# Kernel optimization log

Measured on AMD Instinct MI355X. Metric: run time of the kernel, lower is better.

Reference implementation:

```python
import jax, jax.numpy as jnp
import numpy as np

N_NODES = 100000
N_EDGES = 1600000
N_GRAPHS = 1024
HID = 128
NODE_DIM = 7
EDGE_DIM = 3
LAYERS = 4
LN_EPS = 1e-5


def setup_inputs() -> dict:
    key = jax.random.key(0)
    ks = jax.random.split(key, 24)
    s = lambda i, shape, scale=0.05: (jax.random.normal(ks[i], shape, dtype=jnp.float32) * scale)
    x = jax.random.normal(ks[0], (N_NODES, NODE_DIM), dtype=jnp.float32)
    edge_index = jax.random.randint(ks[1], (2, N_EDGES), 0, N_NODES, dtype=jnp.int32)
    edge_attr = jax.random.normal(ks[2], (N_EDGES, EDGE_DIM), dtype=jnp.float32)
    batch = jnp.sort(jax.random.randint(ks[3], (N_NODES,), 0, N_GRAPHS, dtype=jnp.int32))
    return {
        'x': x, 'edge_index': edge_index, 'edge_attr': edge_attr, 'batch': batch,
        'inW': s(4, (NODE_DIM, HID)), 'inb': s(5, (HID,)),
        'edgeW': s(6, (LAYERS, EDGE_DIM, HID)), 'edgeb': s(7, (LAYERS, HID)),
        'w1': s(8, (LAYERS, HID, HID)), 'b1': s(9, (LAYERS, HID)),
        'w2': s(10, (LAYERS, HID, HID)), 'b2': s(11, (LAYERS, HID)),
        'gamma': jnp.ones((LAYERS, HID), dtype=jnp.float32),
        'beta': jnp.zeros((LAYERS, HID), dtype=jnp.float32),
        'fcW1': s(12, (HID, HID)), 'fcb1': s(13, (HID,)),
        'fcW2': s(14, (HID, HID // 2)), 'fcb2': s(15, (HID // 2,)),
        'fcW3': s(16, (HID // 2, 1)), 'fcb3': s(17, (1,)),
    }


def _layernorm(x, gamma, beta):
    mu = jnp.mean(x, axis=-1, keepdims=True)
    var = jnp.mean(jnp.square(x - mu), axis=-1, keepdims=True)
    return (x - mu) * jax.lax.rsqrt(var + LN_EPS) * gamma + beta


def reference(x, edge_index, edge_attr, batch, inW, inb, edgeW, edgeb,
              w1, b1, w2, b2, gamma, beta, fcW1, fcb1, fcW2, fcb2, fcW3, fcb3):
    src, dst = edge_index[0], edge_index[1]
    h = x @ inW + inb  # [N, HID]
    for l in range(LAYERS):
        e = edge_attr @ edgeW[l] + edgeb[l]              # [E, HID]
        msg = jax.nn.relu(h[src] + e)                    # gather + relu
        agg = jax.ops.segment_sum(msg, dst, num_segments=N_NODES)  # scatter-add
        g = agg + h                                      # (1+eps)*x_r with eps=0
        g = jax.nn.relu(g @ w1[l] + b1[l]) @ w2[l] + b2[l]  # GINE MLP
        h = _layernorm(h + jax.nn.relu(g), gamma[l], beta[l])  # residual + LN
    # global mean pool over graphs
    sums = jax.ops.segment_sum(h, batch, num_segments=N_GRAPHS)
    cnt = jax.ops.segment_sum(jnp.ones((h.shape[0],), h.dtype), batch, num_segments=N_GRAPHS)
    pooled = sums / jnp.maximum(cnt, 1.0)[:, None]
    # head (dropout is identity in eval)
    o = jax.nn.relu(pooled @ fcW1 + fcb1)
    o = jax.nn.relu(o @ fcW2 + fcb2)
    return o @ fcW3 + fcb3  # [N_GRAPHS, 1]
```

## Files before the change

kernel.cpp:

```cpp
#include <hip/hip_runtime.h>

#define N_NODES 100000
#define N_EDGES 1600000
#define N_GRAPHS 1024
#define HID 128
#define LAYERS 4
#define LN_EPS 1e-5f
#define GTS 136
#define HLS 132
#define NB_PROJ 50000
#define NB_WCONV 512
#define NBUCK 1563
#define BCAP 2048
#define NSTREAM 8
#define CURPAD 32
#define EPB 4096
#define NB_BS 391


typedef __attribute__((ext_vector_type(8))) short bf16x8;
typedef __attribute__((ext_vector_type(4))) float f32x4;
typedef __attribute__((ext_vector_type(2))) float f32x2;

__device__ __forceinline__ unsigned short f2bf(float x) {
    unsigned v = __float_as_uint(x);
    return (unsigned short)((v + 0x7fffu + ((v >> 16) & 1u)) >> 16);
}
__device__ __forceinline__ float bfval(unsigned short u) {
    return __uint_as_float((unsigned)u << 16);
}
__device__ __forceinline__ f32x2 pk_fma(f32x2 a, f32x2 b, f32x2 c) {
    f32x2 d;
    asm("v_pk_fma_f32 %0, %1, %2, %3" : "=v"(d) : "v"(a), "v"(b), "v"(c));
    return d;
}
__device__ __forceinline__ f32x2 pk_add(f32x2 a, f32x2 b) {
    f32x2 d;
    asm("v_pk_add_f32 %0, %1, %2" : "=v"(d) : "v"(a), "v"(b));
    return d;
}

__global__ __launch_bounds__(256) void k_prep(
    const float* __restrict__ x, const float* __restrict__ inW,
    const float* __restrict__ inb, float* __restrict__ h,
    unsigned short* __restrict__ hb,
    const float* __restrict__ w1, const float* __restrict__ w2,
    unsigned short* __restrict__ wf_hi, unsigned short* __restrict__ wf_lo) {
    if (blockIdx.x < NB_PROJ) {
        int idx = blockIdx.x * 256 + threadIdx.x;
        int n = idx >> 7, c = idx & 127;
        const float* xr = x + n * 7;
        float s = inb[c];
#pragma unroll
        for (int k = 0; k < 7; ++k) s += xr[k] * inW[k * HID + c];
        h[idx] = s;
        hb[idx] = f2bf(s);
    } else {
        int idx = (blockIdx.x - NB_PROJ) * 256 + threadIdx.x;
        int wid = idx >> 14;
        int layer = wid >> 1, which = wid & 1;
        int within = idx & 16383;
        int nt = within >> 11;
        int ks = (within >> 9) & 3;
        int ln = (within >> 3) & 63;
        int j = within & 7;
        const float* W = (which ? w2 : w1) + layer * HID * HID;
        int k = ks * 32 + (ln >> 4) * 8 + j;
        int n = nt * 16 + (ln & 15);
        float v = W[k * HID + n];
        unsigned short hi = f2bf(v);
        wf_hi[idx] = hi;
        wf_lo[idx] = f2bf(v - bfval(hi));
    }
}

__global__ __launch_bounds__(256) void k_hist(
    const int* __restrict__ ei, int* __restrict__ cnt2) {
    __shared__ int hcnt[NBUCK];
    const int t = threadIdx.x;
    for (int i = t; i < NBUCK; i += 256) hcnt[i] = 0;
    __syncthreads();
    const int e0 = blockIdx.x * EPB;
    const int eend = (e0 + EPB < N_EDGES) ? e0 + EPB : N_EDGES;
#pragma unroll
    for (int k = 0; k < 16; ++k) {
        const int e = e0 + k * 256 + t;
        if (e < eend) atomicAdd(&hcnt[ei[N_EDGES + e] >> 6], 1);
    }
    __syncthreads();
    const int sgrp = blockIdx.x & 7;
    for (int i = t; i < NBUCK; i += 256) {
        const int c = hcnt[i];
        if (c) atomicAdd(&cnt2[((i << 3) + sgrp) << 5], c);
    }
}

__global__ __launch_bounds__(1024) void k_segscan(
    const int* __restrict__ cnt2, int* __restrict__ pcur,
    int* __restrict__ bucket_base, int* __restrict__ row_ptr) {
    __shared__ int lsum[1024];
    const int t = threadIdx.x;
    const int b0 = 2 * t, b1 = 2 * t + 1;
    int u0 = 0, u1 = 0;
    if (b0 < NBUCK) {
#pragma unroll
        for (int s = 0; s < NSTREAM; ++s) u0 += cnt2[((b0 << 3) + s) << 5];
    }
    if (b1 < NBUCK) {
#pragma unroll
        for (int s = 0; s < NSTREAM; ++s) u1 += cnt2[((b1 << 3) + s) << 5];
    }
    const int v = u0 + u1;
    lsum[t] = v;
    __syncthreads();
    for (int off = 1; off < 1024; off <<= 1) {
        const int u = (t >= off) ? lsum[t - off] : 0;
        __syncthreads();
        lsum[t] += u;
        __syncthreads();
    }
    const int excl = lsum[t] - v;
    if (b0 < NBUCK) {
        bucket_base[b0] = excl;
        int run = excl;
#pragma unroll
        for (int s = 0; s < NSTREAM; ++s) {
            const int c = ((b0 << 3) + s) << 5;
            pcur[c] = run;
            run += cnt2[c];
        }
    }
    if (b1 < NBUCK) {
        const int base1 = excl + u0;
        bucket_base[b1] = base1;
        int run = base1;
#pragma unroll
        for (int s = 0; s < NSTREAM; ++s) {
            const int c = ((b1 << 3) + s) << 5;
            pcur[c] = run;
            run += cnt2[c];
        }
    }
    if (t == 0) {
        bucket_base[NBUCK] = N_EDGES;
        row_ptr[N_NODES] = N_EDGES;
    }
}

__global__ __launch_bounds__(256) void k_binscat(
    const int* __restrict__ ei, const float* __restrict__ ea,
    int* __restrict__ pcur, int4* __restrict__ erec) {
    __shared__ int hcnt[NBUCK];
    const int t = threadIdx.x;
    for (int i = t; i < NBUCK; i += 256) hcnt[i] = 0;
    __syncthreads();
    const int e0 = blockIdx.x * EPB;
    const int eend = (e0 + EPB < N_EDGES) ? e0 + EPB : N_EDGES;
#pragma unroll
    for (int k = 0; k < 16; ++k) {
        const int e = e0 + k * 256 + t;
        if (e < eend) atomicAdd(&hcnt[ei[N_EDGES + e] >> 6], 1);
    }
    __syncthreads();
    const int sgrp = blockIdx.x & 7;
    for (int i = t; i < NBUCK; i += 256) {
        const int c = hcnt[i];
        hcnt[i] = c ? atomicAdd(&pcur[((i << 3) + sgrp) << 5], c) : 0;
    }
    __syncthreads();
#pragma unroll
    for (int k = 0; k < 16; ++k) {
        const int e = e0 + k * 256 + t;
        if (e < eend) {
            const int src = ei[e];
            const int dst = ei[N_EDGES + e];
            const float a0 = ea[e * 3 + 0];
            const float a1 = ea[e * 3 + 1];
            const float a2 = ea[e * 3 + 2];
            const int pos = atomicAdd(&hcnt[dst >> 6], 1);
            int4 r;
            r.x = src | ((dst & 63) << 20);
            r.y = __float_as_int(a0);
            r.z = __float_as_int(a1);
            r.w = __float_as_int(a2);
            erec[pos] = r;
        }
    }
}

__global__ __launch_bounds__(256) void k_bucketsort(
    const int4* __restrict__ erec, const int* __restrict__ bucket_base,
    int* __restrict__ row_ptr, int4* __restrict__ edata) {
    __shared__ int rhist[64];
    __shared__ int lcur[64];
    __shared__ int4 stage[BCAP];
    const int b = blockIdx.x;
    const int nb0 = b << 6;
    const int nrows = (nb0 + 64 <= N_NODES) ? 64 : (N_NODES - nb0);
    const int base = bucket_base[b];
    const int end = bucket_base[b + 1];
    const int cnt = end - base;
    const int t = threadIdx.x;
    if (t < 64) rhist[t] = 0;
    __syncthreads();
    for (int i = t; i < cnt; i += 256)
        atomicAdd(&rhist[(erec[base + i].x >> 20) & 63], 1);
    __syncthreads();
    if (t < 64) {
        const int v = rhist[t];
        int incl = v;
#pragma unroll
        for (int off = 1; off < 64; off <<= 1) {
            const int u = __shfl_up(incl, off);
            if (t >= off) incl += u;
        }
        const int excl = incl - v;
        lcur[t] = excl;
        if (t < nrows) row_ptr[nb0 + t] = base + excl;
    }
    __syncthreads();
    if (cnt <= BCAP) {
        for (int i = t; i < cnt; i += 256) {
            const int4 r = erec[base + i];
            stage[atomicAdd(&lcur[(r.x >> 20) & 63], 1)] = r;
        }
        __syncthreads();
        for (int i = t; i < cnt; i += 256) {
            int4 r = stage[i];
            r.x &= 0xFFFFF;
            edata[base + i] = r;
        }
    } else {
        for (int i = t; i < cnt; i += 256) {
            const int4 r = erec[base + i];
            const int pos = base + atomicAdd(&lcur[(r.x >> 20) & 63], 1);
            int4 o = r;
            o.x = r.x & 0xFFFFF;
            edata[pos] = o;
        }
    }
}

#define FLUSHSTEP {                                                            \
    if (rcur == 0)      { a0v = acc2; rnext = rp2; }                           \
    else if (rcur == 1) { a1v = acc2; rnext = rp3; }                           \
    else                { a2v = acc2; rnext = 0x7fffffff; }                    \
    acc2[0] = 0.f; acc2[1] = 0.f; ++rcur; }

#define EL(JJ)                                                                 \
    const int s##JJ = __builtin_amdgcn_readlane(cS, j + JJ);                   \
    const unsigned gq##JJ = *(const unsigned*)(hbin + (long)s##JJ * HID + c2);

#define EC(JJ) {                                                               \
    const int gi = t + j + (JJ);                                               \
    while (gi >= rnext) FLUSHSTEP                                              \
    const f32x4 qq = attAB[j + (JJ)];                                          \
    const f32x2 pC = attC[j + (JJ)];                                           \
    f32x2 pA; pA[0] = qq[0]; pA[1] = qq[1];                                    \
    f32x2 pB; pB[0] = qq[2]; pB[1] = qq[3];                                    \
    f32x2 g2; g2[0] = __uint_as_float(gq##JJ << 16);                           \
    g2[1] = __uint_as_float(gq##JJ & 0xffff0000u);                             \
    const f32x2 m2 = pk_fma(pC, ew2v, pk_fma(pB, ew1v, pk_fma(pA, ew0v,        \
                            pk_add(g2, ebv2))));                               \
    f32x2 r2; r2[0] = fmaxf(m2[0], 0.f); r2[1] = fmaxf(m2[1], 0.f);            \
    acc2 = pk_add(acc2, r2); }

#define ROW_OUT(R, AV) {                                                       \
    const float2 hv = *(const float2*)(h + (long)(nb + (R)) * HID + c2);       \
    *(float2*)&h_lds[(r0 + (R)) * HLS + c2] = hv;                              \
    const float gx = hv.x + (AV)[0], gy = hv.y + (AV)[1];                      \
    const unsigned short hx = f2bf(gx), hy = f2bf(gy);                         \
    const unsigned short lx = f2bf(gx - bfval(hx)), ly = f2bf(gy - bfval(hy)); \
    *(unsigned*)&gt_hi[(r0 + (R)) * GTS + c2] = (unsigned)hx | ((unsigned)hy << 16); \
    *(unsigned*)&gt_lo[(r0 + (R)) * GTS + c2] = (unsigned)lx | ((unsigned)ly << 16); }

#define T1_OUT(CC, NT) {                                                       \
    const float4 bv = *(const float4*)(b1 + (NT) * 16 + q4);                   \
    const float v0 = fmaxf(CC[0] + bv.x, 0.f);                                 \
    const float v1 = fmaxf(CC[1] + bv.y, 0.f);                                 \
    const float v2 = fmaxf(CC[2] + bv.z, 0.f);                                 \
    const float v3 = fmaxf(CC[3] + bv.w, 0.f);                                 \
    const unsigned short h0_ = f2bf(v0), h1_ = f2bf(v1), h2_ = f2bf(v2), h3_ = f2bf(v3); \
    const unsigned short l0_ = f2bf(v0 - bfval(h0_)), l1_ = f2bf(v1 - bfval(h1_)); \
    const unsigned short l2_ = f2bf(v2 - bfval(h2_)), l3_ = f2bf(v3 - bfval(h3_)); \
    *(uint2*)&t1_hi[ln15 * GTS + (NT) * 16 + q4] =                             \
        make_uint2((unsigned)h0_ | ((unsigned)h1_ << 16), (unsigned)h2_ | ((unsigned)h3_ << 16)); \
    *(uint2*)&t1_lo[ln15 * GTS + (NT) * 16 + q4] =                             \
        make_uint2((unsigned)l0_ | ((unsigned)l1_ << 16), (unsigned)l2_ | ((unsigned)l3_ << 16)); }

__global__ __launch_bounds__(256, 8) void k_node_update(
    const int4* __restrict__ edata, const int* __restrict__ row_ptr,
    const float* __restrict__ eW, const float* __restrict__ eb,
    float* __restrict__ h, const unsigned short* __restrict__ hbin,
    unsigned short* __restrict__ hbout,
    const unsigned short* __restrict__ w1f_hi, const unsigned short* __restrict__ w1f_lo,
    const unsigned short* __restrict__ w2f_hi, const unsigned short* __restrict__ w2f_lo,
    const float* __restrict__ b1, const float* __restrict__ b2,
    const float* __restrict__ gamma, const float* __restrict__ beta) {
    __shared__ __align__(16) unsigned char smem[25856];
    float* stats = (float*)smem;
    unsigned short* gt_hi = (unsigned short*)(smem + 0);
    unsigned short* gt_lo = (unsigned short*)(smem + 4352);
    unsigned short* t1_hi = (unsigned short*)(smem + 8704);
    unsigned short* t1_lo = (unsigned short*)(smem + 13056);
    float* h_lds = (float*)(smem + 17408);

    const int wave = threadIdx.x >> 6;
    const int lane = threadIdx.x & 63;
    const int n0 = blockIdx.x * 16;
    const int r0 = wave * 4;
    const int c2 = lane * 2;

    {
        f32x4* attAB = (f32x4*)(smem + 8704 + wave * 1536);
        f32x2* attC  = (f32x2*)(smem + 8704 + wave * 1536 + 1024);
        const f32x2 ew0v = *(const f32x2*)(eW + 0 * HID + c2);
        const f32x2 ew1v = *(const f32x2*)(eW + 1 * HID + c2);
        const f32x2 ew2v = *(const f32x2*)(eW + 2 * HID + c2);
        const f32x2 ebv2 = *(const f32x2*)(eb + c2);
        const int nb = n0 + r0;
        const int rp0 = __builtin_amdgcn_readfirstlane(row_ptr[nb + 0]);
        const int rp1 = __builtin_amdgcn_readfirstlane(row_ptr[nb + 1]);
        const int rp2 = __builtin_amdgcn_readfirstlane(row_ptr[nb + 2]);
        const int rp3 = __builtin_amdgcn_readfirstlane(row_ptr[nb + 3]);
        const int rp4 = __builtin_amdgcn_readfirstlane(row_ptr[nb + 4]);

        f32x2 a0v = {0.f, 0.f}, a1v = {0.f, 0.f};
        f32x2 a2v = {0.f, 0.f}, a3v = {0.f, 0.f};
        f32x2 acc2 = {0.f, 0.f};
        int rcur = 0;
        int rnext = rp1;

        int4 cE = {0, 0, 0, 0}, nE = {0, 0, 0, 0};
        if (rp0 + lane < rp4) cE = edata[rp0 + lane];
        for (int t = rp0; t < rp4; t += 64) {
            const int cnt = (rp4 - t < 64) ? (rp4 - t) : 64;
            f32x4 dAB;
            dAB[0] = __int_as_float(cE.y); dAB[1] = dAB[0];
            dAB[2] = __int_as_float(cE.z); dAB[3] = dAB[2];
            f32x2 dC;
            dC[0] = __int_as_float(cE.w); dC[1] = dC[0];
            attAB[lane] = dAB;
            attC[lane] = dC;
            const int cS = cE.x;
            __builtin_amdgcn_wave_barrier();
            if (t + 64 + lane < rp4)
                nE = edata[t + 64 + lane];
            int j = 0;
            for (; j + 16 <= cnt; j += 16) {
                EL(0) EL(1) EL(2) EL(3) EL(4) EL(5) EL(6) EL(7)
                EL(8) EL(9) EL(10) EL(11) EL(12) EL(13) EL(14) EL(15)
                EC(0) EC(1) EC(2) EC(3) EC(4) EC(5) EC(6) EC(7)
                EC(8) EC(9) EC(10) EC(11) EC(12) EC(13) EC(14) EC(15)
            }
            for (; j + 4 <= cnt; j += 4) {
                EL(0) EL(1) EL(2) EL(3)
                EC(0) EC(1) EC(2) EC(3)
            }
            for (; j < cnt; ++j) {
                EL(0)
                EC(0)
            }
            __builtin_amdgcn_wave_barrier();
            cE = nE;
        }
        if (rcur == 0)      a0v = acc2;
        else if (rcur == 1) a1v = acc2;
        else if (rcur == 2) a2v = acc2;
        else                a3v = acc2;
        ROW_OUT(0, a0v)
        ROW_OUT(1, a1v)
        ROW_OUT(2, a2v)
        ROW_OUT(3, a3v)
    }
    __syncthreads();

    const int ln15 = lane & 15;
    const int q8 = (lane >> 4) * 8;
    const int q4 = (lane >> 4) * 4;
    const int nt0 = wave * 2, nt1 = nt0 + 1;

    {
        f32x4 c0 = {0.f, 0.f, 0.f, 0.f};
        f32x4 c1 = {0.f, 0.f, 0.f, 0.f};
#pragma unroll
        for (int ks = 0; ks < 4; ++ks) {
            const bf16x8 bh = *(const bf16x8*)&gt_hi[ln15 * GTS + ks * 32 + q8];
            const bf16x8 bl = *(const bf16x8*)&gt_lo[ln15 * GTS + ks * 32 + q8];
            const bf16x8 a0h = *(const bf16x8*)(w1f_hi + (((nt0 * 4 + ks) * 64 + lane) << 3));
            const bf16x8 a0l = *(const bf16x8*)(w1f_lo + (((nt0 * 4 + ks) * 64 + lane) << 3));
            const bf16x8 a1h = *(const bf16x8*)(w1f_hi + (((nt1 * 4 + ks) * 64 + lane) << 3));
            const bf16x8 a1l = *(const bf16x8*)(w1f_lo + (((nt1 * 4 + ks) * 64 + lane) << 3));
            c0 = __builtin_amdgcn_mfma_f32_16x16x32_bf16(a0h, bh, c0, 0, 0, 0);
            c0 = __builtin_amdgcn_mfma_f32_16x16x32_bf16(a0h, bl, c0, 0, 0, 0);
            c0 = __builtin_amdgcn_mfma_f32_16x16x32_bf16(a0l, bh, c0, 0, 0, 0);
            c1 = __builtin_amdgcn_mfma_f32_16x16x32_bf16(a1h, bh, c1, 0, 0, 0);
            c1 = __builtin_amdgcn_mfma_f32_16x16x32_bf16(a1h, bl, c1, 0, 0, 0);
            c1 = __builtin_amdgcn_mfma_f32_16x16x32_bf16(a1l, bh, c1, 0, 0, 0);
        }
        T1_OUT(c0, nt0)
        T1_OUT(c1, nt1)
    }
    __syncthreads();

    {
        f32x4 c0 = {0.f, 0.f, 0.f, 0.f};
        f32x4 c1 = {0.f, 0.f, 0.f, 0.f};
#pragma unroll
        for (int ks = 0; ks < 4; ++ks) {
            const bf16x8 bh = *(const bf16x8*)&t1_hi[ln15 * GTS + ks * 32 + q8];
            const bf16x8 bl = *(const bf16x8*)&t1_lo[ln15 * GTS + ks * 32 + q8];
            const bf16x8 a0h = *(const bf16x8*)(w2f_hi + (((nt0 * 4 + ks) * 64 + lane) << 3));
            const bf16x8 a0l = *(const bf16x8*)(w2f_lo + (((nt0 * 4 + ks) * 64 + lane) << 3));
            const bf16x8 a1h = *(const bf16x8*)(w2f_hi + (((nt1 * 4 + ks) * 64 + lane) << 3));
            const bf16x8 a1l = *(const bf16x8*)(w2f_lo + (((nt1 * 4 + ks) * 64 + lane) << 3));
            c0 = __builtin_amdgcn_mfma_f32_16x16x32_bf16(a0h, bh, c0, 0, 0, 0);
            c0 = __builtin_amdgcn_mfma_f32_16x16x32_bf16(a0h, bl, c0, 0, 0, 0);
            c0 = __builtin_amdgcn_mfma_f32_16x16x32_bf16(a0l, bh, c0, 0, 0, 0);
            c1 = __builtin_amdgcn_mfma_f32_16x16x32_bf16(a1h, bh, c1, 0, 0, 0);
            c1 = __builtin_amdgcn_mfma_f32_16x16x32_bf16(a1h, bl, c1, 0, 0, 0);
            c1 = __builtin_amdgcn_mfma_f32_16x16x32_bf16(a1l, bh, c1, 0, 0, 0);
        }
        const int row = n0 + ln15;
        const float4 b20 = *(const float4*)(b2 + nt0 * 16 + q4);
        const float4 b21 = *(const float4*)(b2 + nt1 * 16 + q4);
        const float4 hv0 = *(const float4*)&h_lds[ln15 * HLS + nt0 * 16 + q4];
        const float4 hv1 = *(const float4*)&h_lds[ln15 * HLS + nt1 * 16 + q4];
        float4 u0, u1;
        u0.x = hv0.x + fmaxf(c0[0] + b20.x, 0.f);
        u0.y = hv0.y + fmaxf(c0[1] + b20.y, 0.f);
        u0.z = hv0.z + fmaxf(c0[2] + b20.z, 0.f);
        u0.w = hv0.w + fmaxf(c0[3] + b20.w, 0.f);
        u1.x = hv1.x + fmaxf(c1[0] + b21.x, 0.f);
        u1.y = hv1.y + fmaxf(c1[1] + b21.y, 0.f);
        u1.z = hv1.z + fmaxf(c1[2] + b21.z, 0.f);
        u1.w = hv1.w + fmaxf(c1[3] + b21.w, 0.f);
        float s = u0.x + u0.y + u0.z + u0.w + u1.x + u1.y + u1.z + u1.w;
        float s2 = u0.x * u0.x + u0.y * u0.y + u0.z * u0.z + u0.w * u0.w +
                   u1.x * u1.x + u1.y * u1.y + u1.z * u1.z + u1.w * u1.w;
        s += __shfl_xor(s, 16); s2 += __shfl_xor(s2, 16);
        s += __shfl_xor(s, 32); s2 += __shfl_xor(s2, 32);
        if (lane < 16) {
            stats[wave * 32 + lane * 2 + 0] = s;
            stats[wave * 32 + lane * 2 + 1] = s2;
        }
        __syncthreads();
        const float S  = stats[0 * 32 + ln15 * 2] + stats[1 * 32 + ln15 * 2] +
                         stats[2 * 32 + ln15 * 2] + stats[3 * 32 + ln15 * 2];
        const float S2 = stats[0 * 32 + ln15 * 2 + 1] + stats[1 * 32 + ln15 * 2 + 1] +
                         stats[2 * 32 + ln15 * 2 + 1] + stats[3 * 32 + ln15 * 2 + 1];
        const float mu = S * (1.f / HID);
        const float var = S2 * (1.f / HID) - mu * mu;
        const float inv = rsqrtf(var + LN_EPS);
        const float4 gm0 = *(const float4*)(gamma + nt0 * 16 + q4);
        const float4 gm1 = *(const float4*)(gamma + nt1 * 16 + q4);
        const float4 bt0 = *(const float4*)(beta + nt0 * 16 + q4);
        const float4 bt1 = *(const float4*)(beta + nt1 * 16 + q4);
        float4 o0, o1;
        o0.x = (u0.x - mu) * inv * gm0.x + bt0.x;
        o0.y = (u0.y - mu) * inv * gm0.y + bt0.y;
        o0.z = (u0.z - mu) * inv * gm0.z + bt0.z;
        o0.w = (u0.w - mu) * inv * gm0.w + bt0.w;
        o1.x = (u1.x - mu) * inv * gm1.x + bt1.x;
        o1.y = (u1.y - mu) * inv * gm1.y + bt1.y;
        o1.z = (u1.z - mu) * inv * gm1.z + bt1.z;
        o1.w = (u1.w - mu) * inv * gm1.w + bt1.w;
        *(float4*)(h + (long)row * HID + nt0 * 16 + q4) = o0;
        *(float4*)(h + (long)row * HID + nt1 * 16 + q4) = o1;
        *(uint2*)(hbout + (long)row * HID + nt0 * 16 + q4) =
            make_uint2((unsigned)f2bf(o0.x) | ((unsigned)f2bf(o0.y) << 16),
                       (unsigned)f2bf(o0.z) | ((unsigned)f2bf(o0.w) << 16));
        *(uint2*)(hbout + (long)row * HID + nt1 * 16 + q4) =
            make_uint2((unsigned)f2bf(o1.x) | ((unsigned)f2bf(o1.y) << 16),
                       (unsigned)f2bf(o1.z) | ((unsigned)f2bf(o1.w) << 16));
    }
}

__global__ __launch_bounds__(128) void k_pool(
    const float* __restrict__ h, const int* __restrict__ batch,
    float* __restrict__ sums, float* __restrict__ cnt) {
    const int c = threadIdx.x;
    const int n0 = blockIdx.x * 64;
    if (n0 >= N_NODES) return;
    const int nend = min(n0 + 64, N_NODES);
    int cur = batch[n0];
    float acc = 0.f;
    int runlen = 0;
    for (int n = n0; n < nend; ++n) {
        const int b = batch[n];
        if (b != cur) {
            atomicAdd(&sums[(long)cur * HID + c], acc);
            if (c == 0) atomicAdd(&cnt[cur], (float)runlen);
            acc = 0.f;
            runlen = 0;
            cur = b;
        }
        acc += h[(long)n * HID + c];
        ++runlen;
    }
    atomicAdd(&sums[(long)cur * HID + c], acc);
    if (c == 0) atomicAdd(&cnt[cur], (float)runlen);
}

__global__ __launch_bounds__(128) void k_head(
    const float* __restrict__ sums, const float* __restrict__ cnt,
    const float* __restrict__ fcW1, const float* __restrict__ fcb1,
    const float* __restrict__ fcW2, const float* __restrict__ fcb2,
    const float* __restrict__ fcW3, const float* __restrict__ fcb3,
    float* __restrict__ out) {
    __shared__ float p[HID];
    __shared__ float o1[HID];
    __shared__ float o2[64];
    const int g = blockIdx.x, t = threadIdx.x;
    const float c = fmaxf(cnt[g], 1.0f);
    p[t] = sums[g * HID + t] / c;
    __syncthreads();
    float s = fcb1[t];
    for (int k = 0; k < HID; ++k) s += p[k] * fcW1[k * HID + t];
    o1[t] = fmaxf(s, 0.f);
    __syncthreads();
    if (t < 64) {
        float s2 = fcb2[t];
        for (int k = 0; k < HID; ++k) s2 += o1[k] * fcW2[k * 64 + t];
        o2[t] = fmaxf(s2, 0.f);
    }
    __syncthreads();
    if (t < 64) {
        float v = o2[t] * fcW3[t];
#pragma unroll
        for (int off = 32; off > 0; off >>= 1) v += __shfl_down(v, off);
        if (t == 0) out[g] = v + fcb3[0];
    }
}

extern "C" void kernel_launch(void* const* d_in, const int* in_sizes, int n_in,
                              void* d_out, int out_size, void* d_ws, size_t ws_size,
                              hipStream_t stream) {
    const float* x    = (const float*)d_in[0];
    const int*   ei   = (const int*)d_in[1];
    const float* ea   = (const float*)d_in[2];
    const int*   batch= (const int*)d_in[3];
    const float* inW  = (const float*)d_in[4];
    const float* inb  = (const float*)d_in[5];
    const float* edgeW= (const float*)d_in[6];
    const float* edgeb= (const float*)d_in[7];
    const float* w1   = (const float*)d_in[8];
    const float* b1   = (const float*)d_in[9];
    const float* w2   = (const float*)d_in[10];
    const float* b2   = (const float*)d_in[11];
    const float* gamma= (const float*)d_in[12];
    const float* beta = (const float*)d_in[13];
    const float* fcW1 = (const float*)d_in[14];
    const float* fcb1 = (const float*)d_in[15];
    const float* fcW2 = (const float*)d_in[16];
    const float* fcb2 = (const float*)d_in[17];
    const float* fcW3 = (const float*)d_in[18];
    const float* fcb3 = (const float*)d_in[19];
    float* out = (float*)d_out;

    int4*  edata = (int4*)d_ws;
    float* h     = (float*)(edata + (size_t)N_EDGES);
    unsigned short* hb0 = (unsigned short*)(h + (size_t)N_NODES * HID);
    unsigned short* hb1 = hb0 + (size_t)N_NODES * HID;
    unsigned short* wf_hi = hb1 + (size_t)N_NODES * HID;
    unsigned short* wf_lo = wf_hi + LAYERS * 2 * 16384;
    int*    row_ptr = (int*)(wf_lo + LAYERS * 2 * 16384);
    int*    pcur    = (int*)(((size_t)(row_ptr + (N_NODES + 1)) + 127) & ~(size_t)127);
    int*    bucket_base = pcur + NBUCK * NSTREAM * CURPAD;
    int*    cnt2    = (int*)(((size_t)(bucket_base + NBUCK + 1) + 127) & ~(size_t)127);
    float*  sums    = (float*)(cnt2 + NBUCK * NSTREAM * CURPAD);
    float*  cnt     = sums + (size_t)N_GRAPHS * HID;
    const size_t zbytes = (size_t)NBUCK * NSTREAM * CURPAD * sizeof(int) +
                          ((size_t)N_GRAPHS * HID + N_GRAPHS) * sizeof(float);
    int4*   erec    = (int4*)hb1;

    hipMemsetAsync(cnt2, 0, zbytes, stream);

    k_prep<<<NB_PROJ + NB_WCONV, 256, 0, stream>>>(x, inW, inb, h, hb0,
                                                   w1, w2, wf_hi, wf_lo);

    k_hist<<<NB_BS, 256, 0, stream>>>(ei, cnt2);
    k_segscan<<<1, 1024, 0, stream>>>(cnt2, pcur, bucket_base, row_ptr);
    k_binscat<<<NB_BS, 256, 0, stream>>>(ei, ea, pcur, erec);
    k_bucketsort<<<NBUCK, 256, 0, stream>>>(erec, bucket_base, row_ptr, edata);

    unsigned short* hbin = hb0;
    unsigned short* hbout = hb1;
    for (int l = 0; l < LAYERS; ++l) {
        k_node_update<<<N_NODES / 16, 256, 0, stream>>>(
            edata, row_ptr, edgeW + l * 3 * HID, edgeb + l * HID,
            h, hbin, hbout,
            wf_hi + (l * 2 + 0) * 16384, wf_lo + (l * 2 + 0) * 16384,
            wf_hi + (l * 2 + 1) * 16384, wf_lo + (l * 2 + 1) * 16384,
            b1 + l * HID, b2 + l * HID, gamma + l * HID, beta + l * HID);
        unsigned short* tmp = hbin; hbin = hbout; hbout = tmp;
    }

    k_pool<<<(N_NODES + 63) / 64, 128, 0, stream>>>(h, batch, sums, cnt);
    k_head<<<N_GRAPHS, 128, 0, stream>>>(sums, cnt, fcW1, fcb1, fcW2, fcb2,
                                         fcW3, fcb3, out);
}
```

Before: 692.2 us.

## Replace atomic bucket cursors with per-block histogram and column scan

The edge binning now writes a full per-block bucket histogram, scans each bucket's counts across blocks in a new kernel, and gives binscat precomputed per-block offsets. This removes the global atomic cursors and the second histogram pass inside binscat. In exchange it adds a kernel launch and a block-by-bucket histogram buffer in workspace. The cross-block order is permuted (t%49*8 + t/49), which makes placement deterministic, but the order is arbitrary and only needs to be consistent.

```diff
diff --git a/kernel.cpp b/kernel.cpp
--- a/kernel.cpp
+++ b/kernel.cpp
@@ -12,8 +12,6 @@
 #define NB_WCONV 512
 #define NBUCK 1563
 #define BCAP 2048
-#define NSTREAM 8
-#define CURPAD 32
 #define EPB 4096
 #define NB_BS 391
 
@@ -75,7 +73,7 @@
 }
 
 __global__ __launch_bounds__(256) void k_hist(
-    const int* __restrict__ ei, int* __restrict__ cnt2) {
+    const int* __restrict__ ei, int* __restrict__ Xpb) {
     __shared__ int hcnt[NBUCK];
     const int t = threadIdx.x;
     for (int i = t; i < NBUCK; i += 256) hcnt[i] = 0;
@@ -88,28 +86,40 @@
         if (e < eend) atomicAdd(&hcnt[ei[N_EDGES + e] >> 6], 1);
     }
     __syncthreads();
-    const int sgrp = blockIdx.x & 7;
-    for (int i = t; i < NBUCK; i += 256) {
-        const int c = hcnt[i];
-        if (c) atomicAdd(&cnt2[((i << 3) + sgrp) << 5], c);
-    }
+    for (int i = t; i < NBUCK; i += 256)
+        Xpb[blockIdx.x * NBUCK + i] = hcnt[i];
+}
+
+__global__ __launch_bounds__(512) void k_bscan(
+    const int* __restrict__ Xpb, int* __restrict__ lexcl,
+    int* __restrict__ T) {
+    __shared__ int tmp[512];
+    const int b = blockIdx.x;
+    const int t = threadIdx.x;
+    int blk = -1;
+    if (t < 343)        blk = (t % 49) * 8 + (t / 49);
+    else if (t < NB_BS) blk = (t - 343) * 8 + 7;
+    const int v = (blk >= 0) ? Xpb[blk * NBUCK + b] : 0;
+    tmp[t] = v;
+    __syncthreads();
+    for (int off = 1; off < 512; off <<= 1) {
+        const int u = (t >= off) ? tmp[t - off] : 0;
+        __syncthreads();
+        tmp[t] += u;
+        __syncthreads();
+    }
+    if (blk >= 0) lexcl[b * NB_BS + blk] = tmp[t] - v;
+    if (t == 511) T[b] = tmp[511];
 }
 
 __global__ __launch_bounds__(1024) void k_segscan(
-    const int* __restrict__ cnt2, int* __restrict__ pcur,
-    int* __restrict__ bucket_base, int* __restrict__ row_ptr) {
+    const int* __restrict__ T, int* __restrict__ bucket_base,
+    int* __restrict__ row_ptr) {
     __shared__ int lsum[1024];
     const int t = threadIdx.x;
     const int b0 = 2 * t, b1 = 2 * t + 1;
-    int u0 = 0, u1 = 0;
-    if (b0 < NBUCK) {
-#pragma unroll
-        for (int s = 0; s < NSTREAM; ++s) u0 += cnt2[((b0 << 3) + s) << 5];
-    }
-    if (b1 < NBUCK) {
-#pragma unroll
-        for (int s = 0; s < NSTREAM; ++s) u1 += cnt2[((b1 << 3) + s) << 5];
-    }
+    const int u0 = (b0 < NBUCK) ? T[b0] : 0;
+    const int u1 = (b1 < NBUCK) ? T[b1] : 0;
     const int v = u0 + u1;
     lsum[t] = v;
     __syncthreads();
@@ -120,27 +130,8 @@
         __syncthreads();
     }
     const int excl = lsum[t] - v;
-    if (b0 < NBUCK) {
-        bucket_base[b0] = excl;
-        int run = excl;
-#pragma unroll
-        for (int s = 0; s < NSTREAM; ++s) {
-            const int c = ((b0 << 3) + s) << 5;
-            pcur[c] = run;
-            run += cnt2[c];
-        }
-    }
-    if (b1 < NBUCK) {
-        const int base1 = excl + u0;
-        bucket_base[b1] = base1;
-        int run = base1;
-#pragma unroll
-        for (int s = 0; s < NSTREAM; ++s) {
-            const int c = ((b1 << 3) + s) << 5;
-            pcur[c] = run;
-            run += cnt2[c];
-        }
-    }
+    if (b0 < NBUCK) bucket_base[b0] = excl;
+    if (b1 < NBUCK) bucket_base[b1] = excl + u0;
     if (t == 0) {
         bucket_base[NBUCK] = N_EDGES;
         row_ptr[N_NODES] = N_EDGES;
@@ -149,25 +140,16 @@
 
 __global__ __launch_bounds__(256) void k_binscat(
     const int* __restrict__ ei, const float* __restrict__ ea,
-    int* __restrict__ pcur, int4* __restrict__ erec) {
-    __shared__ int hcnt[NBUCK];
+    const int* __restrict__ bucket_base, const int* __restrict__ lexcl,
+    int4* __restrict__ erec) {
+    __shared__ int lcur[NBUCK];
     const int t = threadIdx.x;
-    for (int i = t; i < NBUCK; i += 256) hcnt[i] = 0;
-    __syncthreads();
-    const int e0 = blockIdx.x * EPB;
+    const int blk = blockIdx.x;
+    for (int i = t; i < NBUCK; i += 256)
+        lcur[i] = bucket_base[i] + lexcl[i * NB_BS + blk];
+    __syncthreads();
+    const int e0 = blk * EPB;
     const int eend = (e0 + EPB < N_EDGES) ? e0 + EPB : N_EDGES;
-#pragma unroll
-    for (int k = 0; k < 16; ++k) {
-        const int e = e0 + k * 256 + t;
-        if (e < eend) atomicAdd(&hcnt[ei[N_EDGES + e] >> 6], 1);
-    }
-    __syncthreads();
-    const int sgrp = blockIdx.x & 7;
-    for (int i = t; i < NBUCK; i += 256) {
-        const int c = hcnt[i];
-        hcnt[i] = c ? atomicAdd(&pcur[((i << 3) + sgrp) << 5], c) : 0;
-    }
-    __syncthreads();
 #pragma unroll
     for (int k = 0; k < 16; ++k) {
         const int e = e0 + k * 256 + t;
@@ -177,7 +159,7 @@
             const float a0 = ea[e * 3 + 0];
             const float a1 = ea[e * 3 + 1];
             const float a2 = ea[e * 3 + 2];
-            const int pos = atomicAdd(&hcnt[dst >> 6], 1);
+            const int pos = atomicAdd(&lcur[dst >> 6], 1);
             int4 r;
             r.x = src | ((dst & 63) << 20);
             r.y = __float_as_int(a0);
@@ -565,23 +547,24 @@
     unsigned short* wf_hi = hb1 + (size_t)N_NODES * HID;
     unsigned short* wf_lo = wf_hi + LAYERS * 2 * 16384;
     int*    row_ptr = (int*)(wf_lo + LAYERS * 2 * 16384);
-    int*    pcur    = (int*)(((size_t)(row_ptr + (N_NODES + 1)) + 127) & ~(size_t)127);
-    int*    bucket_base = pcur + NBUCK * NSTREAM * CURPAD;
-    int*    cnt2    = (int*)(((size_t)(bucket_base + NBUCK + 1) + 127) & ~(size_t)127);
-    float*  sums    = (float*)(cnt2 + NBUCK * NSTREAM * CURPAD);
+    int*    bucket_base = row_ptr + (N_NODES + 1);
+    int*    T       = bucket_base + (NBUCK + 1);
+    float*  sums    = (float*)(T + NBUCK);
     float*  cnt     = sums + (size_t)N_GRAPHS * HID;
-    const size_t zbytes = (size_t)NBUCK * NSTREAM * CURPAD * sizeof(int) +
-                          ((size_t)N_GRAPHS * HID + N_GRAPHS) * sizeof(float);
+    const size_t zbytes = ((size_t)N_GRAPHS * HID + N_GRAPHS) * sizeof(float);
+    int*    Xpb     = (int*)edata;
+    int*    lexcl   = Xpb + (size_t)NB_BS * NBUCK;
     int4*   erec    = (int4*)hb1;
 
-    hipMemsetAsync(cnt2, 0, zbytes, stream);
+    hipMemsetAsync(sums, 0, zbytes, stream);
 
     k_prep<<<NB_PROJ + NB_WCONV, 256, 0, stream>>>(x, inW, inb, h, hb0,
                                                    w1, w2, wf_hi, wf_lo);
 
-    k_hist<<<NB_BS, 256, 0, stream>>>(ei, cnt2);
-    k_segscan<<<1, 1024, 0, stream>>>(cnt2, pcur, bucket_base, row_ptr);
-    k_binscat<<<NB_BS, 256, 0, stream>>>(ei, ea, pcur, erec);
+    k_hist<<<NB_BS, 256, 0, stream>>>(ei, Xpb);
+    k_bscan<<<NBUCK, 512, 0, stream>>>(Xpb, lexcl, T);
+    k_segscan<<<1, 1024, 0, stream>>>(T, bucket_base, row_ptr);
+    k_binscat<<<NB_BS, 256, 0, stream>>>(ei, ea, bucket_base, lexcl, erec);
     k_bucketsort<<<NBUCK, 256, 0, stream>>>(erec, bucket_base, row_ptr, edata);
 
     unsigned short* hbin = hb0;
```

Result: faster. 647.2 us (-6.5%).
